# Performance work log

Hardware: AMD Instinct MI355X
Metric: run time of the kernel (lower is better)

The kernel has to match this reference:

```python
import jax, jax.numpy as jnp
import numpy as np

T, I, H, C = 2048, 1024, 1024, 1000


def _lstm(x, W_ih, W_hh, b_ih, b_hh):
    # x: [T, I]; PyTorch LSTM gate order: i, f, g, o
    x_proj = x @ W_ih.T + b_ih + b_hh  # [T, 4H] input projection hoisted out of scan
    h_dim = W_hh.shape[1]

    def step(carry, xp):
        h, c = carry
        gates = xp + h @ W_hh.T  # [4H]
        i, f, g, o = jnp.split(gates, 4)
        i = jax.nn.sigmoid(i)
        f = jax.nn.sigmoid(f)
        g = jnp.tanh(g)
        o = jax.nn.sigmoid(o)
        c_new = f * c + i * g
        h_new = o * jnp.tanh(c_new)
        return (h_new, c_new), h_new

    h0 = jnp.zeros((h_dim,), x.dtype)
    (_, _), hs = jax.lax.scan(step, (h0, h0), x_proj)
    return hs  # [T, H]


def setup_inputs() -> dict:
    key = jax.random.key(0)
    ks = jax.random.split(key, 12)
    s = 1.0 / np.sqrt(H)  # torch LSTM uniform(-1/sqrt(H), 1/sqrt(H)) scale
    u = lambda k, shape: jax.random.uniform(k, shape, jnp.float32, -s, s)
    return {
        "x": jax.random.normal(ks[0], (T, I), jnp.float32),
        "W_ih_f": u(ks[1], (4 * H, I)),
        "W_hh_f": u(ks[2], (4 * H, H)),
        "b_ih_f": u(ks[3], (4 * H,)),
        "b_hh_f": u(ks[4], (4 * H,)),
        "W_ih_b": u(ks[5], (4 * H, I)),
        "W_hh_b": u(ks[6], (4 * H, H)),
        "b_ih_b": u(ks[7], (4 * H,)),
        "b_hh_b": u(ks[8], (4 * H,)),
        "fc_W": u(ks[9], (C, 2 * H)),
        "fc_b": u(ks[10], (C,)),
    }


def reference(x, W_ih_f, W_hh_f, b_ih_f, b_hh_f, W_ih_b, W_hh_b, b_ih_b, b_hh_b, fc_W, fc_b):
    h_fwd = _lstm(x, W_ih_f, W_hh_f, b_ih_f, b_hh_f)            # [T, H]
    h_bwd = _lstm(x[::-1], W_ih_b, W_hh_b, b_ih_b, b_hh_b)[::-1]  # [T, H], re-reversed
    h = jnp.concatenate([h_fwd, h_bwd], axis=-1)                  # [T, 2H]
    return h @ fc_W.T + fc_b                                      # [T, C]
```

## Files before the change

### kernel.cpp

```cpp
#include <hip/hip_runtime.h>
#include <hip/hip_bf16.h>
#include <cstdint>


typedef __fp16 h2 __attribute__((ext_vector_type(2)));
typedef __fp16 h8 __attribute__((ext_vector_type(8)));
typedef float f4 __attribute__((ext_vector_type(4)));
typedef unsigned long long u64;

#define T_LEN 2048

static __device__ __forceinline__ unsigned int packh2(float a, float b) {
  h2 r = __builtin_amdgcn_cvt_pkrtz(a, b);
  return __builtin_bit_cast(unsigned int, r);
}
static __device__ __forceinline__ float fdot2u(unsigned int a, unsigned int b, float c) {
  return __builtin_amdgcn_fdot2(__builtin_bit_cast(h2, a), __builtin_bit_cast(h2, b), c, false);
}
static __device__ __forceinline__ float sigmoidf_(float x) {
  return 1.f / (1.f + __expf(-x));
}
static __device__ __forceinline__ float tanhf_(float x) {
  float e = __expf(-2.f * fabsf(x));
  float r = (1.f - e) / (1.f + e);
  return copysignf(r, x);
}
static __device__ __forceinline__ u64 aload(const u64* p) {
  return __hip_atomic_load(p, __ATOMIC_RELAXED, __HIP_MEMORY_SCOPE_AGENT);
}

#define DPP_ADD1(v, CTRL)                                                      \
  v += __builtin_bit_cast(                                                     \
      float, __builtin_amdgcn_update_dpp(0, __builtin_bit_cast(int, v), CTRL,  \
                                         0xf, 0xf, true))
#define DPP_ROUND(CTRL)                                                        \
  DPP_ADD1(acc0, CTRL);                                                        \
  DPP_ADD1(acc1, CTRL);                                                        \
  DPP_ADD1(acc2, CTRL);                                                        \
  DPP_ADD1(acc3, CTRL)

__global__ void convert_all(const float* __restrict__ x, const float* __restrict__ wf,
                            const float* __restrict__ wb, const float* __restrict__ fcw,
                            _Float16* __restrict__ xf, _Float16* __restrict__ wff,
                            _Float16* __restrict__ wbf, _Float16* __restrict__ fcwf) {
  const size_t SX = 2097152, SW = 4194304, SFC = 2097152;
  size_t i = (size_t)blockIdx.x * 256 + threadIdx.x;
  if (i < SX) {
    xf[i] = (_Float16)x[i];
  } else if (i < SX + SW) {
    size_t j = i - SX; wff[j] = (_Float16)wf[j];
  } else if (i < SX + 2 * SW) {
    size_t j = i - SX - SW; wbf[j] = (_Float16)wb[j];
  } else if (i < SX + 2 * SW + SFC) {
    size_t j = i - SX - 2 * SW;
    int row = (int)(j >> 11), col = (int)(j & 2047);
    fcwf[j] = (row < 1000) ? (_Float16)fcw[(size_t)row * 2048 + col] : (_Float16)0.f;
  }
}

__global__ void init_state(u64* __restrict__ hc, unsigned* __restrict__ ep) {
  __shared__ unsigned sbs;
  if (threadIdx.x == 0) sbs = atomicAdd(ep, 1u) << 12;
  __syncthreads();
  u64 v = (u64)sbs;
  for (int i = threadIdx.x; i < 2048; i += 256)
    __hip_atomic_store(&hc[i], v, __ATOMIC_RELAXED, __HIP_MEMORY_SCOPE_AGENT);
}

#define LSTR 80

template <int MODE>
__global__ __launch_bounds__(256, 2) void gemm_f16(
    const _Float16* __restrict__ A, const _Float16* __restrict__ B,
    const float* __restrict__ bias1, const float* __restrict__ bias2,
    void* __restrict__ Cout, int M, int N, int K, int nout, int rev) {
  __shared__ _Float16 As[128 * LSTR];
  __shared__ _Float16 Bs[128 * LSTR];

  const int tid = threadIdx.x;
  const int ntn = N >> 7;
  const int tm = blockIdx.x / ntn, tn = blockIdx.x % ntn;
  const int wid = tid >> 6, lane = tid & 63;
  const int wr = wid >> 1, wc = wid & 1;
  const int quad = lane >> 4, l16 = lane & 15;

  const int srow = tid >> 1, seg = tid & 1;
  const int arow = rev ? (M - 1 - (tm * 128 + srow)) : (tm * 128 + srow);
  const int brow = tn * 128 + srow;

  f4 acc[4][4];
#pragma unroll
  for (int i = 0; i < 4; ++i)
#pragma unroll
    for (int j = 0; j < 4; ++j) acc[i][j] = (f4)0.f;

  for (int k0 = 0; k0 < K; k0 += 64) {
    uint4 va[4], vb[4];
    const uint4* gpa = (const uint4*)(A + (size_t)arow * K + k0 + seg * 32);
    const uint4* gpb = (const uint4*)(B + (size_t)brow * K + k0 + seg * 32);
#pragma unroll
    for (int c = 0; c < 4; ++c) va[c] = gpa[c];
#pragma unroll
    for (int c = 0; c < 4; ++c) vb[c] = gpb[c];

    __syncthreads();
    uint4* lpa = (uint4*)&As[srow * LSTR + seg * 32];
    uint4* lpb = (uint4*)&Bs[srow * LSTR + seg * 32];
#pragma unroll
    for (int c = 0; c < 4; ++c) lpa[c] = va[c];
#pragma unroll
    for (int c = 0; c < 4; ++c) lpb[c] = vb[c];
    __syncthreads();

#pragma unroll
    for (int kk = 0; kk < 64; kk += 32) {
      h8 af[4], bf[4];
#pragma unroll
      for (int i = 0; i < 4; ++i) {
        int m = wr * 64 + i * 16 + l16;
        af[i] = *(const h8*)&As[m * LSTR + kk + quad * 8];
        int n = wc * 64 + i * 16 + l16;
        bf[i] = *(const h8*)&Bs[n * LSTR + kk + quad * 8];
      }
#pragma unroll
      for (int i = 0; i < 4; ++i)
#pragma unroll
        for (int j = 0; j < 4; ++j)
          acc[i][j] = __builtin_amdgcn_mfma_f32_16x16x32_f16(af[i], bf[j], acc[i][j], 0, 0, 0);
    }
  }

  const int cm0 = tm * 128 + wr * 64, cn0 = tn * 128 + wc * 64;
#pragma unroll
  for (int i = 0; i < 4; ++i) {
#pragma unroll
    for (int j = 0; j < 4; ++j) {
      int n = cn0 + j * 16 + l16;
#pragma unroll
      for (int r = 0; r < 4; ++r) {
        int m = cm0 + i * 16 + quad * 4 + r;
        float v = acc[i][j][r];
        if (MODE == 0) {
          v += bias1[n] + bias2[n];
          ((_Float16*)Cout)[(size_t)m * N + n] = (_Float16)v;
        } else {
          if (n < nout) ((float*)Cout)[(size_t)m * nout + n] = v + bias1[n];
        }
      }
    }
  }
}

__global__ __launch_bounds__(256, 1) void lstm_rec(
    const float* __restrict__ Whh_f, const float* __restrict__ Whh_b,
    const _Float16* __restrict__ xp,
    u64* __restrict__ hc,
    unsigned* __restrict__ ep,
    _Float16* __restrict__ hhist) {
  const int tid = threadIdx.x;
  const int blk = blockIdx.x;
  const int dir = blk >> 6;
  const int ib = blk & 63;
  const int j0 = ib * 16;
  const int wv = tid >> 6;
  const int l = tid & 63;
  const int rr = l >> 4;
  const int kq = l & 15;
  const int wrow_u = j0 + 4 * wv + rr;

  const unsigned SB =
      (__hip_atomic_load(ep, __ATOMIC_RELAXED, __HIP_MEMORY_SCOPE_AGENT) - 1u) << 12;

  const float* Whh = dir ? Whh_b : Whh_f;
  const _Float16* xpd = xp + (size_t)dir * (2048u * 4096u);

  __shared__ unsigned int lds_h[2][16 * 36];

  unsigned int w[4][32];
#pragma unroll
  for (int g = 0; g < 4; ++g) {
    const float* wp = Whh + (size_t)(g * 1024 + wrow_u) * 1024 + kq * 64;
#pragma unroll
    for (int i = 0; i < 16; ++i) {
      float4 v = ((const float4*)wp)[i];
      w[g][2 * i] = packh2(v.x, v.y);
      w[g][2 * i + 1] = packh2(v.z, v.w);
    }
  }

  float c = 0.f;

  float xf0, xf1, xf2, xf3;
  {
    const _Float16* xr = xpd + wrow_u;
    xf0 = (float)xr[0]; xf1 = (float)xr[1024];
    xf2 = (float)xr[2048]; xf3 = (float)xr[3072];
  }

  for (int t = 0; t < T_LEN; ++t) {
    const int buf = t & 1;
    const unsigned exp0 = SB + (unsigned)t;

    const u64* src = hc + (((size_t)buf * 2 + dir) * 512 + 2 * tid);
    u64 a = aload(&src[0]);
    u64 b = aload(&src[1]);

    int tnx = (t + 1 < T_LEN) ? t + 1 : t;
    const _Float16* xr = xpd + (size_t)tnx * 4096 + wrow_u;
    _Float16 n0 = xr[0], n1 = xr[1024], n2 = xr[2048], n3 = xr[3072];

    unsigned d0, d1;
    {
      int cnt = 0;
      while ((unsigned)a != exp0 || (unsigned)b != exp0) {
        if (++cnt > (1 << 12)) break;
        a = aload(&src[0]);
        b = aload(&src[1]);
      }
      d0 = (unsigned)(a >> 32);
      d1 = (unsigned)(b >> 32);
    }

    *(uint2*)&lds_h[buf][(tid >> 4) * 36 + 2 * (tid & 15)] = make_uint2(d0, d1);
    __syncthreads();

    float acc0 = 0.f, acc1 = 0.f, acc2 = 0.f, acc3 = 0.f;
    const uint4* hp = (const uint4*)&lds_h[buf][kq * 36];
#pragma unroll
    for (int i = 0; i < 8; ++i) {
      uint4 hv = hp[i];
      acc0 = fdot2u(w[0][4 * i + 0], hv.x, acc0);
      acc0 = fdot2u(w[0][4 * i + 1], hv.y, acc0);
      acc0 = fdot2u(w[0][4 * i + 2], hv.z, acc0);
      acc0 = fdot2u(w[0][4 * i + 3], hv.w, acc0);
      acc1 = fdot2u(w[1][4 * i + 0], hv.x, acc1);
      acc1 = fdot2u(w[1][4 * i + 1], hv.y, acc1);
      acc1 = fdot2u(w[1][4 * i + 2], hv.z, acc1);
      acc1 = fdot2u(w[1][4 * i + 3], hv.w, acc1);
      acc2 = fdot2u(w[2][4 * i + 0], hv.x, acc2);
      acc2 = fdot2u(w[2][4 * i + 1], hv.y, acc2);
      acc2 = fdot2u(w[2][4 * i + 2], hv.z, acc2);
      acc2 = fdot2u(w[2][4 * i + 3], hv.w, acc2);
      acc3 = fdot2u(w[3][4 * i + 0], hv.x, acc3);
      acc3 = fdot2u(w[3][4 * i + 1], hv.y, acc3);
      acc3 = fdot2u(w[3][4 * i + 2], hv.z, acc3);
      acc3 = fdot2u(w[3][4 * i + 3], hv.w, acc3);
    }
    DPP_ROUND(0xB1);
    DPP_ROUND(0x4E);
    DPP_ROUND(0x141);
    DPP_ROUND(0x140);

    float ii = sigmoidf_(acc0 + xf0);
    float ff = sigmoidf_(acc1 + xf1);
    float g_ = tanhf_(acc2 + xf2);
    float oo = sigmoidf_(acc3 + xf3);
    c = ff * c + ii * g_;
    float h = oo * tanhf_(c);

    float hx = __shfl_xor(h, 16, 64);
    unsigned pk = packh2(h, hx);
    unsigned pko = (unsigned)__shfl_xor((int)pk, 32, 64);

    const unsigned tg = SB + (unsigned)(t + 1);
    const int slot = (t + 1) & 1;
    if (l < 2) {
      u64 v = (l == 0) ? (((u64)pk << 32) | tg) : (((u64)pko << 32) | tg);
      u64* dst = hc + (((size_t)slot * 2 + dir) * 512 +
                       (size_t)(ib * 8 + 2 * wv + l));
      (void)__hip_atomic_exchange(dst, v, __ATOMIC_RELAXED,
                                  __HIP_MEMORY_SCOPE_AGENT);
      int tout = dir ? (T_LEN - 1 - t) : t;
      *(unsigned*)&hhist[(size_t)tout * 2048 +
                         (size_t)(dir * 1024 + j0 + 4 * wv + 2 * l)] =
          (l == 0) ? pk : pko;
    }

    xf0 = (float)n0; xf1 = (float)n1; xf2 = (float)n2; xf3 = (float)n3;
  }
}

extern "C" void kernel_launch(void* const* d_in, const int* in_sizes, int n_in,
                              void* d_out, int out_size, void* d_ws, size_t ws_size,
                              hipStream_t stream) {
  (void)in_sizes; (void)n_in; (void)out_size; (void)ws_size;
  const float* x     = (const float*)d_in[0];
  const float* Wih_f = (const float*)d_in[1];
  const float* Whh_f = (const float*)d_in[2];
  const float* bih_f = (const float*)d_in[3];
  const float* bhh_f = (const float*)d_in[4];
  const float* Wih_b = (const float*)d_in[5];
  const float* Whh_b = (const float*)d_in[6];
  const float* bih_b = (const float*)d_in[7];
  const float* bhh_b = (const float*)d_in[8];
  const float* fcW   = (const float*)d_in[9];
  const float* fcb   = (const float*)d_in[10];

  char* ws = (char*)d_ws;
  _Float16* xf16   = (_Float16*)(ws + 0);
  _Float16* wih16f = (_Float16*)(ws + 4194304);
  _Float16* wih16b = (_Float16*)(ws + 12582912);
  _Float16* fcw16  = (_Float16*)(ws + 20971520);
  _Float16* xp16   = (_Float16*)(ws + 25165824);
  _Float16* hhist  = (_Float16*)(ws + 58720256);
  u64*      hc     = (u64*)     (ws + 67108864);
  unsigned* epoch  = (unsigned*)(ws + 67141632);

  const size_t SX = 2097152, SW = 4194304, SFC = 2097152;
  const size_t total_cvt = SX + 2 * SW + SFC;

  convert_all<<<dim3((unsigned)((total_cvt + 255) / 256)), 256, 0, stream>>>(
      x, Wih_f, Wih_b, fcW, xf16, wih16f, wih16b, fcw16);
  init_state<<<1, 256, 0, stream>>>(hc, epoch);

  gemm_f16<0><<<dim3(512), 256, 0, stream>>>(xf16, wih16f, bih_f, bhh_f,
                                             (void*)xp16, 2048, 4096, 1024, 4096, 0);
  gemm_f16<0><<<dim3(512), 256, 0, stream>>>(xf16, wih16b, bih_b, bhh_b,
                                             (void*)(xp16 + (size_t)2048 * 4096),
                                             2048, 4096, 1024, 4096, 1);

  lstm_rec<<<dim3(128), 256, 0, stream>>>(Whh_f, Whh_b, xp16, hc, epoch, hhist);

  gemm_f16<1><<<dim3(128), 256, 0, stream>>>(hhist, fcw16, fcb, nullptr,
                                             d_out, 2048, 1024, 2048, 1000, 0);
}
```

Baseline: 3.337 ms.

## Pipeline recurrent h polling with overlapped wide loads and interleave gate projections

The input-projection GEMM now writes its output with the four gates interleaved per hidden unit, so the recurrent kernel fetches the next step's four gate inputs with one 8-byte load instead of four scattered halves. The spin-wait on the exchanged hidden state is rewritten with inline-asm 16-byte coherent loads, keeping two polls in flight alternately and falling back to the original atomic loop after a bounded count. __syncthreads is replaced with an explicit lgkmcnt wait plus s_barrier. This targets the per-timestep latency of the cross-block handoff, which is the serial critical path. In exchange it adds hand-written asm and waitcnt ordering that is fragile, and it relies on the two 8-byte fields being read together in one wide load.

```diff
diff --git a/kernel.cpp b/kernel.cpp
--- a/kernel.cpp
+++ b/kernel.cpp
@@ -6,6 +6,7 @@
 typedef __fp16 h2 __attribute__((ext_vector_type(2)));
 typedef __fp16 h8 __attribute__((ext_vector_type(8)));
 typedef float f4 __attribute__((ext_vector_type(4)));
+typedef unsigned int u32x4 __attribute__((ext_vector_type(4)));
 typedef unsigned long long u64;
 
 #define T_LEN 2048
@@ -142,7 +143,8 @@
         float v = acc[i][j][r];
         if (MODE == 0) {
           v += bias1[n] + bias2[n];
-          ((_Float16*)Cout)[(size_t)m * N + n] = (_Float16)v;
+          int cc = ((n & 1023) << 2) | (n >> 10);
+          ((_Float16*)Cout)[(size_t)m * N + cc] = (_Float16)v;
         } else {
           if (n < nout) ((float*)Cout)[(size_t)m * nout + n] = v + bias1[n];
         }
@@ -192,37 +194,65 @@
 
   float xf0, xf1, xf2, xf3;
   {
-    const _Float16* xr = xpd + wrow_u;
-    xf0 = (float)xr[0]; xf1 = (float)xr[1024];
-    xf2 = (float)xr[2048]; xf3 = (float)xr[3072];
+    uint2 xv = *(const uint2*)(xpd + (size_t)wrow_u * 4);
+    h2 xa = __builtin_bit_cast(h2, xv.x);
+    h2 xb = __builtin_bit_cast(h2, xv.y);
+    xf0 = (float)xa[0]; xf1 = (float)xa[1];
+    xf2 = (float)xb[0]; xf3 = (float)xb[1];
   }
 
   for (int t = 0; t < T_LEN; ++t) {
     const int buf = t & 1;
     const unsigned exp0 = SB + (unsigned)t;
-
     const u64* src = hc + (((size_t)buf * 2 + dir) * 512 + 2 * tid);
-    u64 a = aload(&src[0]);
-    u64 b = aload(&src[1]);
-
     int tnx = (t + 1 < T_LEN) ? t + 1 : t;
-    const _Float16* xr = xpd + (size_t)tnx * 4096 + wrow_u;
-    _Float16 n0 = xr[0], n1 = xr[1024], n2 = xr[2048], n3 = xr[3072];
+    const _Float16* xr = xpd + (size_t)tnx * 4096 + (size_t)wrow_u * 4;
+
+    u32x4 A, Bv;
+    uint2 XP;
+    asm volatile("global_load_dwordx4 %0, %1, off sc0 sc1"
+                 : "=v"(A) : "v"(src) : "memory");
+    asm volatile("global_load_dwordx2 %0, %1, off"
+                 : "=v"(XP) : "v"(xr) : "memory");
+    asm volatile("global_load_dwordx4 %0, %1, off sc0 sc1"
+                 : "=v"(Bv) : "v"(src) : "memory");
 
     unsigned d0, d1;
     {
       int cnt = 0;
-      while ((unsigned)a != exp0 || (unsigned)b != exp0) {
-        if (++cnt > (1 << 12)) break;
-        a = aload(&src[0]);
-        b = aload(&src[1]);
+      for (;;) {
+        asm volatile("s_waitcnt vmcnt(1)" ::: "memory");
+        __builtin_amdgcn_sched_barrier(0);
+        if (A[0] == exp0 && A[2] == exp0) { d0 = A[1]; d1 = A[3]; break; }
+        asm volatile("global_load_dwordx4 %0, %1, off sc0 sc1"
+                     : "=v"(A) : "v"(src) : "memory");
+        asm volatile("s_waitcnt vmcnt(1)" ::: "memory");
+        __builtin_amdgcn_sched_barrier(0);
+        if (Bv[0] == exp0 && Bv[2] == exp0) { d0 = Bv[1]; d1 = Bv[3]; break; }
+        asm volatile("global_load_dwordx4 %0, %1, off sc0 sc1"
+                     : "=v"(Bv) : "v"(src) : "memory");
+        if (++cnt > 32) {
+          u64 a = aload(&src[0]), b = aload(&src[1]);
+          int c2 = 0;
+          while ((unsigned)a != exp0 || (unsigned)b != exp0) {
+            if (++c2 > (1 << 12)) break;
+            a = aload(&src[0]);
+            b = aload(&src[1]);
+          }
+          d0 = (unsigned)(a >> 32);
+          d1 = (unsigned)(b >> 32);
+          break;
+        }
       }
-      d0 = (unsigned)(a >> 32);
-      d1 = (unsigned)(b >> 32);
-    }
+    }
+
+    h2 xa = __builtin_bit_cast(h2, XP.x);
+    h2 xb = __builtin_bit_cast(h2, XP.y);
+    float nf0 = (float)xa[0], nf1 = (float)xa[1];
+    float nf2 = (float)xb[0], nf3 = (float)xb[1];
 
     *(uint2*)&lds_h[buf][(tid >> 4) * 36 + 2 * (tid & 15)] = make_uint2(d0, d1);
-    __syncthreads();
+    asm volatile("s_waitcnt lgkmcnt(0)\n\ts_barrier" ::: "memory");
 
     float acc0 = 0.f, acc1 = 0.f, acc2 = 0.f, acc3 = 0.f;
     const uint4* hp = (const uint4*)&lds_h[buf][kq * 36];
@@ -262,6 +292,9 @@
     unsigned pk = packh2(h, hx);
     unsigned pko = (unsigned)__shfl_xor((int)pk, 32, 64);
 
+    asm volatile("s_waitcnt vmcnt(0)" : : "v"(A), "v"(Bv) : "memory");
+    __builtin_amdgcn_sched_barrier(0);
+
     const unsigned tg = SB + (unsigned)(t + 1);
     const int slot = (t + 1) & 1;
     if (l < 2) {
@@ -276,7 +309,7 @@
           (l == 0) ? pk : pko;
     }
 
-    xf0 = (float)n0; xf1 = (float)n1; xf2 = (float)n2; xf3 = (float)n3;
+    xf0 = nf0; xf1 = nf1; xf2 = nf2; xf3 = nf3;
   }
 }
 
```

Result: slower. 4.996 ms (+49.7%).
